# Performance work log

Hardware: AMD Instinct MI355X
Metric: run time of the kernel (lower is better)

The kernel has to match this reference:

```python
import jax, jax.numpy as jnp
import numpy as np

K = 5           # kernel_size from kernel_kwargs
P = K // 2      # padding (same-size output)
MASK_TH = 0.5   # mask_th init kwarg
EPS = 1e-6

# squared distance of each of the K*K taps from the kernel center, shape [K*K]
_R2 = jnp.asarray(np.array([(dy - P) ** 2 + (dx - P) ** 2
                            for dy in range(K) for dx in range(K)], dtype=np.float32))


def setup_inputs() -> dict:
    key = jax.random.key(0)
    k1, k2 = jax.random.split(key)
    bev_map = jax.random.normal(k1, (4, 1, 768, 768), dtype=jnp.float32)
    # per-pixel scales in [0.5, 2.0) -- realistic kernel bandwidths
    bev_scale = 0.5 + 1.5 * jax.random.uniform(k2, (4, 1, 768, 768), dtype=jnp.float32)
    return {"bev_map": bev_map, "bev_scale": bev_scale}


def reference(bev_map, bev_scale):
    B, C, H, W = bev_map.shape
    x = jax.nn.relu(bev_map)                                   # non_neg = ReLU
    xp = jnp.pad(x, ((0, 0), (0, 0), (P, P), (P, P)))
    # unfold: [B, C, K*K, H, W] shifted views of the padded map
    patches = jnp.stack([xp[:, :, dy:dy + H, dx:dx + W]
                         for dy in range(K) for dx in range(K)], axis=2)
    # ScaleAdaptiveExpKernel: Gaussian weights from per-pixel scale
    # w: [B, 1, K*K, H, W]
    w = jnp.exp(-_R2[None, None, :, None, None]
                / (2.0 * jnp.square(bev_scale)[:, :, None] + EPS))
    bev_map_conv = jnp.sum(patches * w, axis=2)                # [B, C, H, W]
    mask = (bev_map_conv >= MASK_TH).astype(bev_map_conv.dtype)
    return bev_map_conv, mask
```

## Files before the change

kernel.cpp:

```cpp
#include <hip/hip_runtime.h>

#define HH 768
#define WW 768
#define BC 4
#define NPIX (BC * HH * WW)

typedef float f4 __attribute__((ext_vector_type(4)));
typedef float f2 __attribute__((ext_vector_type(2)));

__global__ __launch_bounds__(256) void conv_thresh_kernel(
    const float* __restrict__ bev_map,
    const float* __restrict__ bev_scale,
    float* __restrict__ out)
{
    const int tx = threadIdx.x;
    const int ty = threadIdx.y;
    const int x0 = (blockIdx.x * 64 + tx) * 4;
    const int y0 = blockIdx.y * 8 + ty * 2;
    const int b  = blockIdx.z;

    const size_t plane = (size_t)b * (HH * WW);
    const float* __restrict__ m = bev_map + plane;

    float h0[6][4], h1[6][4], h2[6][4];

#pragma unroll
    for (int r = 0; r < 6; ++r) {
        const int yy = y0 - 2 + r;
        const bool yok = (unsigned)yy < (unsigned)HH;
        const float* rowp = m + yy * WW + x0;
        f4 t;
        if (yok) {
            t = *(const f4*)rowp;
            t.x = fmaxf(t.x, 0.f); t.y = fmaxf(t.y, 0.f);
            t.z = fmaxf(t.z, 0.f); t.w = fmaxf(t.w, 0.f);
        } else {
            t.x = 0.f; t.y = 0.f; t.z = 0.f; t.w = 0.f;
        }
        float lz = __shfl_up(t.z, 1);
        float lw = __shfl_up(t.w, 1);
        float rx = __shfl_down(t.x, 1);
        float ry = __shfl_down(t.y, 1);
        if (tx == 0) {
            lz = 0.f; lw = 0.f;
            if (yok && x0 != 0) {
                f2 t2 = *(const f2*)(rowp - 2);
                lz = fmaxf(t2.x, 0.f); lw = fmaxf(t2.y, 0.f);
            }
        }
        if (tx == 63) {
            rx = 0.f; ry = 0.f;
            if (yok && x0 != WW - 4) {
                f2 t2 = *(const f2*)(rowp + 4);
                rx = fmaxf(t2.x, 0.f); ry = fmaxf(t2.y, 0.f);
            }
        }
        const float w0 = lz, w1 = lw, w2 = t.x, w3 = t.y,
                    w4 = t.z, w5 = t.w, w6 = rx, w7 = ry;
        h0[r][0] = w2; h1[r][0] = w1 + w3; h2[r][0] = w0 + w4;
        h0[r][1] = w3; h1[r][1] = w2 + w4; h2[r][1] = w1 + w5;
        h0[r][2] = w4; h1[r][2] = w3 + w5; h2[r][2] = w2 + w6;
        h0[r][3] = w5; h1[r][3] = w4 + w6; h2[r][3] = w3 + w7;
    }

#pragma unroll
    for (int k = 0; k < 2; ++k) {
        const int oy = y0 + k;
        const size_t idx = plane + (size_t)oy * WW + x0;
        const f4 scv = *(const f4*)(bev_scale + idx);
        f4 conv, mask;
#pragma unroll
        for (int j = 0; j < 4; ++j) {
            const float c0 = h0[k + 2][j];
            const float s1 = h1[k + 2][j] + h0[k + 1][j] + h0[k + 3][j];
            const float s2 = h1[k + 1][j] + h1[k + 3][j];
            const float s4 = h2[k + 2][j] + h0[k][j]     + h0[k + 4][j];
            const float s5 = h2[k + 1][j] + h2[k + 3][j] + h1[k][j] + h1[k + 4][j];
            const float s8 = h2[k][j]     + h2[k + 4][j];

            const float sc = scv[j];
            const float t1 = -1.0f / (2.0f * sc * sc + 1e-6f);
            const float e1 = __expf(t1);
            const float e2 = e1 * e1;
            const float e4 = e2 * e2;
            const float e5 = e4 * e1;
            const float e8 = e4 * e4;

            float cv = c0;
            cv = fmaf(e1, s1, cv);
            cv = fmaf(e2, s2, cv);
            cv = fmaf(e4, s4, cv);
            cv = fmaf(e5, s5, cv);
            cv = fmaf(e8, s8, cv);
            conv[j] = cv;
            mask[j] = (cv >= 0.5f) ? 1.0f : 0.0f;
        }
        *(f4*)(out + idx) = conv;
        *(f4*)(out + idx + (size_t)NPIX) = mask;
    }
}

extern "C" void kernel_launch(void* const* d_in, const int* in_sizes, int n_in,
                              void* d_out, int out_size, void* d_ws, size_t ws_size,
                              hipStream_t stream) {
    const float* bev_map   = (const float*)d_in[0];
    const float* bev_scale = (const float*)d_in[1];
    float* out = (float*)d_out;

    dim3 block(64, 4, 1);
    dim3 grid(WW / 256, HH / 8, BC);
    conv_thresh_kernel<<<grid, block, 0, stream>>>(bev_map, bev_scale, out);
}
```

Measured before the change: 76.44 us.

## Remap blocks to XCD-contiguous strips and hoist scale loads early

Flattens the grid to a 1D launch and remaps block IDs so each of the 8 XCDs, which receive blocks round-robin, processes contiguous row strips. Vertically adjacent blocks then share halo rows in the same L2. The two bev_scale row loads are also issued at kernel start so their latency overlaps the map loads. The mapping hardcodes the grid to 1152 blocks and 8 XCDs, so it only fits this shape.

```diff
diff --git a/kernel.cpp b/kernel.cpp
--- a/kernel.cpp
+++ b/kernel.cpp
@@ -13,14 +13,27 @@
     const float* __restrict__ bev_scale,
     float* __restrict__ out)
 {
+    const int id  = blockIdx.x;
+    const int xcd = id & 7;
+    const int j   = id >> 3;
+    const int strip_global  = xcd * 4 + (j / 36);
+    const int pos = j % 36;
+    const int bz  = strip_global >> 3;
+    const int sip = strip_global & 7;
+    const int bx  = pos % 3;
+    const int by  = sip * 12 + pos / 3;
+
     const int tx = threadIdx.x;
     const int ty = threadIdx.y;
-    const int x0 = (blockIdx.x * 64 + tx) * 4;
-    const int y0 = blockIdx.y * 8 + ty * 2;
-    const int b  = blockIdx.z;
+    const int x0 = (bx * 64 + tx) * 4;
+    const int y0 = by * 8 + ty * 2;
 
-    const size_t plane = (size_t)b * (HH * WW);
+    const size_t plane = (size_t)bz * (HH * WW);
     const float* __restrict__ m = bev_map + plane;
+
+    const size_t idx0 = plane + (size_t)y0 * WW + x0;
+    const f4 scv0 = *(const f4*)(bev_scale + idx0);
+    const f4 scv1 = *(const f4*)(bev_scale + idx0 + WW);
 
     float h0[6][4], h1[6][4], h2[6][4];
 
@@ -65,20 +78,19 @@
 
 #pragma unroll
     for (int k = 0; k < 2; ++k) {
-        const int oy = y0 + k;
-        const size_t idx = plane + (size_t)oy * WW + x0;
-        const f4 scv = *(const f4*)(bev_scale + idx);
+        const size_t idx = idx0 + (size_t)k * WW;
+        const f4 scv = (k == 0) ? scv0 : scv1;
         f4 conv, mask;
 #pragma unroll
-        for (int j = 0; j < 4; ++j) {
-            const float c0 = h0[k + 2][j];
-            const float s1 = h1[k + 2][j] + h0[k + 1][j] + h0[k + 3][j];
-            const float s2 = h1[k + 1][j] + h1[k + 3][j];
-            const float s4 = h2[k + 2][j] + h0[k][j]     + h0[k + 4][j];
-            const float s5 = h2[k + 1][j] + h2[k + 3][j] + h1[k][j] + h1[k + 4][j];
-            const float s8 = h2[k][j]     + h2[k + 4][j];
+        for (int jj = 0; jj < 4; ++jj) {
+            const float c0 = h0[k + 2][jj];
+            const float s1 = h1[k + 2][jj] + h0[k + 1][jj] + h0[k + 3][jj];
+            const float s2 = h1[k + 1][jj] + h1[k + 3][jj];
+            const float s4 = h2[k + 2][jj] + h0[k][jj]     + h0[k + 4][jj];
+            const float s5 = h2[k + 1][jj] + h2[k + 3][jj] + h1[k][jj] + h1[k + 4][jj];
+            const float s8 = h2[k][jj]     + h2[k + 4][jj];
 
-            const float sc = scv[j];
+            const float sc = scv[jj];
             const float t1 = -1.0f / (2.0f * sc * sc + 1e-6f);
             const float e1 = __expf(t1);
             const float e2 = e1 * e1;
@@ -92,8 +104,8 @@
             cv = fmaf(e4, s4, cv);
             cv = fmaf(e5, s5, cv);
             cv = fmaf(e8, s8, cv);
-            conv[j] = cv;
-            mask[j] = (cv >= 0.5f) ? 1.0f : 0.0f;
+            conv[jj] = cv;
+            mask[jj] = (cv >= 0.5f) ? 1.0f : 0.0f;
         }
         *(f4*)(out + idx) = conv;
         *(f4*)(out + idx + (size_t)NPIX) = mask;
@@ -108,6 +120,6 @@
     float* out = (float*)d_out;
 
     dim3 block(64, 4, 1);
-    dim3 grid(WW / 256, HH / 8, BC);
+    dim3 grid(1152, 1, 1);
     conv_thresh_kernel<<<grid, block, 0, stream>>>(bev_map, bev_scale, out);
 }
```

Result: slower. 78.07 us (+2.1%).
